# Optimization experiments

Hardware: AMD Instinct MI355X
Metric: run time of the kernel (lower is better)

Reference implementation:

```python
import jax, jax.numpy as jnp
import numpy as np

B, N, IN_DIM, OUT_DIM, H = 8, 1024, 512, 512, 8
SUP = OUT_DIM // H  # support_dim per head = 64


def setup_inputs() -> dict:
    key = jax.random.key(0)
    ks = jax.random.split(key, 6)
    # 0/1 dense adjacency with self-loops so no row is fully masked
    A = jax.random.randint(ks[0], (B, N, N), 0, 2).astype(jnp.float32)
    A = jnp.maximum(A, jnp.eye(N, dtype=jnp.float32)[None])
    X = jax.random.normal(ks[1], (B, N, IN_DIM), dtype=jnp.float32)
    # parameters, uniform(-1/sqrt(fan_last), 1/sqrt(fan_last)) as in reset_parameters
    sw = 1.0 / np.sqrt(SUP)
    W = jax.random.uniform(ks[2], (H, IN_DIM, SUP), minval=-sw, maxval=sw, dtype=jnp.float32)
    w1 = jax.random.uniform(ks[3], (H, SUP), minval=-sw, maxval=sw, dtype=jnp.float32)
    w2 = jax.random.uniform(ks[4], (H, SUP), minval=-sw, maxval=sw, dtype=jnp.float32)
    b = jax.random.uniform(ks[5], (2, H), minval=-1.0, maxval=1.0, dtype=jnp.float32)
    b1, b2 = b[0], b[1]
    return {"A": A, "X": X, "W": W, "w1": w1, "b1": b1, "w2": w2, "b2": b2}


def reference(A, X, W, w1, b1, w2, b2):
    # per-head projection: [B,H,N,SUP]
    inputs = jnp.einsum('bni,hio->bhno', X, W)
    # additive attention logits: self_fc [B,H,N,1] + neigh_fc [B,H,1,N]
    self_fc = jnp.einsum('bhno,ho->bhn', inputs, w1) + b1[None, :, None]
    neigh_fc = jnp.einsum('bhno,ho->bhn', inputs, w2) + b2[None, :, None]
    logits = jax.nn.leaky_relu(self_fc[..., :, None] + neigh_fc[..., None, :], 0.01)
    mask = -1e9 * (1.0 - A)  # [B,N,N]
    alphas = jax.nn.softmax(logits + mask[:, None], axis=-1)  # [B,H,N,N]
    out = jnp.einsum('bhnm,bhmo->bhno', alphas, inputs)
    out = jax.nn.relu(out)  # default activation = torch.relu
    # concat heads on last dim (head i contiguous), matching torch.cat
    return out.transpose(0, 2, 1, 3).reshape(B, N, H * SUP)
```

## Files before the change

kernel.cpp:

```cpp
#include <hip/hip_runtime.h>
#include <hip/hip_fp16.h>

#define BB 8
#define NN 1024
#define IN_DIM 512
#define HH 8
#define SUP 64
#define HS (HH * SUP)

typedef _Float16 half8 __attribute__((ext_vector_type(8)));
typedef float floatx4 __attribute__((ext_vector_type(4)));

__global__ __launch_bounds__(256) void k0_transpose_w(const float* __restrict__ W,
                                                      _Float16* __restrict__ Wt) {
    __shared__ float tile[64][65];
    const int it = blockIdx.x;
    const int h  = blockIdx.y;
    const int t  = threadIdx.x;

    {
        const int i  = t >> 2;
        const int o0 = (t & 3) * 16;
        const float* src = W + ((size_t)h * IN_DIM + it * 64 + i) * SUP + o0;
#pragma unroll
        for (int j = 0; j < 4; j++) {
            float4 v = ((const float4*)src)[j];
            tile[i][o0 + j * 4 + 0] = v.x;
            tile[i][o0 + j * 4 + 1] = v.y;
            tile[i][o0 + j * 4 + 2] = v.z;
            tile[i][o0 + j * 4 + 3] = v.w;
        }
    }
    __syncthreads();
    {
        const int o  = t >> 2;
        const int i0 = (t & 3) * 16;
        _Float16 buf[16];
#pragma unroll
        for (int j = 0; j < 16; j++) buf[j] = (_Float16)tile[i0 + j][o];
        _Float16* dst = Wt + ((size_t)h * SUP + o) * IN_DIM + it * 64 + i0;
        *(half8*)dst       = *(half8*)buf;
        *(half8*)(dst + 8) = *(half8*)(buf + 8);
    }
}

__global__ __launch_bounds__(256) void k1_proj(const float* __restrict__ X,
                                               const _Float16* __restrict__ Wt,
                                               _Float16* __restrict__ Pt) {
    __shared__ __align__(16) _Float16 xs[64 * 40];
    __shared__ __align__(16) _Float16 wsh[64 * 40];
    __shared__ __align__(16) _Float16 po[64 * 72];

    const int bh = blockIdx.y;
    const int b  = bh >> 3;
    const int h  = bh & 7;
    const int n0 = blockIdx.x * 64;
    const int t    = threadIdx.x;
    const int wave = t >> 6;
    const int lane = t & 63;
    const int quad = lane >> 4;
    const int l15  = lane & 15;
    const int row  = t >> 2;
    const int koff = (t & 3) * 8;

    floatx4 acc[4];
#pragma unroll
    for (int i = 0; i < 4; i++) acc[i] = {0.f, 0.f, 0.f, 0.f};

    const float*    xbase = X + ((size_t)b * NN + n0 + row) * IN_DIM;
    const _Float16* wbase = Wt + ((size_t)h * SUP + row) * IN_DIM;

    for (int k0 = 0; k0 < IN_DIM; k0 += 32) {
        {
            const float* src = xbase + k0 + koff;
            float4 xa = ((const float4*)src)[0];
            float4 xb = ((const float4*)src)[1];
            _Float16 xh[8] = {(_Float16)xa.x, (_Float16)xa.y, (_Float16)xa.z, (_Float16)xa.w,
                              (_Float16)xb.x, (_Float16)xb.y, (_Float16)xb.z, (_Float16)xb.w};
            *(half8*)&xs[row * 40 + koff] = *(half8*)xh;
        }
        {
            *(half8*)&wsh[row * 40 + koff] = *(const half8*)(wbase + k0 + koff);
        }
        __syncthreads();
        half8 af = *(const half8*)&xs[(wave * 16 + l15) * 40 + quad * 8];
#pragma unroll
        for (int ct = 0; ct < 4; ct++) {
            half8 bf = *(const half8*)&wsh[(ct * 16 + l15) * 40 + quad * 8];
            acc[ct] = __builtin_amdgcn_mfma_f32_16x16x32_f16(af, bf, acc[ct], 0, 0, 0);
        }
        __syncthreads();
    }

#pragma unroll
    for (int ct = 0; ct < 4; ct++) {
#pragma unroll
        for (int r = 0; r < 4; r++) {
            int o = ct * 16 + l15;
            int n = wave * 16 + quad * 4 + r;
            po[o * 72 + n] = (_Float16)acc[ct][r];
        }
    }
    __syncthreads();
    {
        const int o   = t >> 2;
        const int nof = (t & 3) * 16;
        _Float16* dst = Pt + ((size_t)bh * SUP + o) * NN + n0 + nof;
        *(half8*)dst       = *(const half8*)&po[o * 72 + nof];
        *(half8*)(dst + 8) = *(const half8*)&po[o * 72 + nof + 8];
    }
}

__global__ __launch_bounds__(256) void k1s_st(const _Float16* __restrict__ Pt,
                                              const float* __restrict__ w1,
                                              const float* __restrict__ b1,
                                              const float* __restrict__ w2,
                                              const float* __restrict__ b2,
                                              float* __restrict__ s_g,
                                              float* __restrict__ t_g,
                                              float* __restrict__ tmax4) {
    const int q  = blockIdx.x;
    const int bh = blockIdx.y;
    const int h  = bh & 7;
    const int t  = threadIdx.x;
    const int n  = q * 256 + t;

    __shared__ float w1s[64], w2s[64];
    __shared__ float red[256];
    if (t < 64) w1s[t] = w1[h * 64 + t];
    else if (t < 128) w2s[t - 64] = w2[h * 64 + (t - 64)];
    __syncthreads();

    const _Float16* base = Pt + (size_t)bh * SUP * NN + n;
    float sa = 0.f, ta = 0.f;
#pragma unroll
    for (int o = 0; o < 64; o++) {
        float p = (float)base[(size_t)o * NN];
        sa += p * w1s[o];
        ta += p * w2s[o];
    }
    sa += b1[h];
    ta += b2[h];
    s_g[(size_t)bh * NN + n] = sa;
    t_g[(size_t)bh * NN + n] = ta;

    red[t] = ta;
    __syncthreads();
    for (int off = 128; off > 0; off >>= 1) {
        if (t < off) red[t] = fmaxf(red[t], red[t + off]);
        __syncthreads();
    }
    if (t == 0) tmax4[bh * 4 + q] = red[0];
}

__global__ __launch_bounds__(256) void k2_attn(const float* __restrict__ A,
                                               const _Float16* __restrict__ Pt,
                                               const float* __restrict__ s_g,
                                               const float* __restrict__ t_g,
                                               const float* __restrict__ tmax4,
                                               float* __restrict__ out) {
    __shared__ __align__(16) _Float16 vts[64 * 40];
    __shared__ __align__(16) _Float16 als[64 * 40];
    __shared__ __align__(16) float tl[NN];
    __shared__ float sl[64], cl[64];
    __shared__ float zred[256];
    __shared__ float zinv[64];

    const int bh = blockIdx.y;
    const int b  = bh >> 3;
    const int h  = bh & 7;
    const int n0 = blockIdx.x * 64;
    const int t    = threadIdx.x;
    const int wave = t >> 6;
    const int lane = t & 63;
    const int quad = lane >> 4;
    const int l15  = lane & 15;
    const int row  = t >> 2;
    const int mg   = t & 3;

    const float tmax = fmaxf(fmaxf(tmax4[bh * 4 + 0], tmax4[bh * 4 + 1]),
                             fmaxf(tmax4[bh * 4 + 2], tmax4[bh * 4 + 3]));

    ((float4*)tl)[t] = ((const float4*)(t_g + (size_t)bh * NN))[t];
    if (t < 64) {
        float sv = s_g[(size_t)bh * NN + n0 + t];
        sl[t] = sv;
        float x = sv + tmax;
        cl[t] = x > 0.f ? x : 0.01f * x;
    }
    __syncthreads();

    floatx4 acc[4];
#pragma unroll
    for (int i = 0; i < 4; i++) acc[i] = {0.f, 0.f, 0.f, 0.f};
    float zp = 0.f;

    const float*    abase = A + ((size_t)b * NN + n0 + row) * NN + mg * 8;
    const _Float16* pbase = Pt + ((size_t)bh * SUP + row) * NN + mg * 8;

    for (int m0 = 0; m0 < NN; m0 += 32) {
        *(half8*)&vts[row * 40 + mg * 8] = *(const half8*)(pbase + m0);

        {
            const float* ap = abase + m0;
            float4 a0 = ((const float4*)ap)[0];
            float4 a1 = ((const float4*)ap)[1];
            float av[8] = {a0.x, a0.y, a0.z, a0.w, a1.x, a1.y, a1.z, a1.w};
            const float sv = sl[row];
            const float c  = cl[row];
            _Float16 wbuf[8];
#pragma unroll
            for (int j = 0; j < 8; j++) {
                float x = sv + tl[m0 + mg * 8 + j];
                float l = x > 0.f ? x : 0.01f * x;
                float e = __expf(l - c);
                float w = av[j] * e;
                zp += w;
                wbuf[j] = (_Float16)w;
            }
            *(half8*)&als[row * 40 + mg * 8] = *(half8*)wbuf;
        }
        __syncthreads();

        half8 af = *(const half8*)&als[(wave * 16 + l15) * 40 + quad * 8];
#pragma unroll
        for (int ct = 0; ct < 4; ct++) {
            half8 bf = *(const half8*)&vts[(ct * 16 + l15) * 40 + quad * 8];
            acc[ct] = __builtin_amdgcn_mfma_f32_16x16x32_f16(af, bf, acc[ct], 0, 0, 0);
        }
        __syncthreads();
    }

    zred[t] = zp;
    __syncthreads();
    if (t < 64) {
        float z = zred[t * 4] + zred[t * 4 + 1] + zred[t * 4 + 2] + zred[t * 4 + 3];
        zinv[t] = 1.0f / z;
    }
    __syncthreads();

#pragma unroll
    for (int r = 0; r < 4; r++) {
        const int rr = wave * 16 + quad * 4 + r;
        const float rz = zinv[rr];
#pragma unroll
        for (int ct = 0; ct < 4; ct++) {
            float v = acc[ct][r] * rz;
            v = v > 0.f ? v : 0.f;
            out[((size_t)b * NN + n0 + rr) * HS + h * SUP + ct * 16 + l15] = v;
        }
    }
}

extern "C" void kernel_launch(void* const* d_in, const int* in_sizes, int n_in,
                              void* d_out, int out_size, void* d_ws, size_t ws_size,
                              hipStream_t stream) {
    const float* A  = (const float*)d_in[0];
    const float* X  = (const float*)d_in[1];
    const float* W  = (const float*)d_in[2];
    const float* w1 = (const float*)d_in[3];
    const float* b1 = (const float*)d_in[4];
    const float* w2 = (const float*)d_in[5];
    const float* b2 = (const float*)d_in[6];
    float* out = (float*)d_out;

    char* ws = (char*)d_ws;
    _Float16* Wt    = (_Float16*)(ws);
    _Float16* Pt    = (_Float16*)(ws + 524288);
    float*    s_g   = (float*)(ws + 524288 + 8388608);
    float*    t_g   = (float*)(ws + 524288 + 8388608 + 262144);
    float*    tmax4 = (float*)(ws + 524288 + 8388608 + 2 * 262144);

    hipLaunchKernelGGL(k0_transpose_w, dim3(IN_DIM / 64, HH), dim3(256), 0, stream, W, Wt);
    hipLaunchKernelGGL(k1_proj, dim3(NN / 64, BB * HH), dim3(256), 0, stream, X, Wt, Pt);
    hipLaunchKernelGGL(k1s_st, dim3(4, BB * HH), dim3(256), 0, stream,
                       Pt, w1, b1, w2, b2, s_g, t_g, tmax4);
    hipLaunchKernelGGL(k2_attn, dim3(NN / 64, BB * HH), dim3(256), 0, stream,
                       A, Pt, s_g, t_g, tmax4, out);
}
```

Baseline: 157.2 us.

## Bit-pack adjacency mask, fuse score projection into GEMM, restructure attention loop

Result: faster. 140.6 us (-10.6%).

```diff
diff --git a/kernel.cpp b/kernel.cpp
--- a/kernel.cpp
+++ b/kernel.cpp
@@ -17,7 +17,6 @@
     const int it = blockIdx.x;
     const int h  = blockIdx.y;
     const int t  = threadIdx.x;
-
     {
         const int i  = t >> 2;
         const int o0 = (t & 3) * 16;
@@ -44,12 +43,36 @@
     }
 }
 
+__global__ __launch_bounds__(256) void kpack(const float* __restrict__ A,
+                                             unsigned char* __restrict__ Am) {
+    const int gw   = blockIdx.x * 4 + (threadIdx.x >> 6);
+    const int lane = threadIdx.x & 63;
+    const float* arow = A + (size_t)gw * NN;
+    unsigned long long keep = 0;
+#pragma unroll
+    for (int g = 0; g < 16; g++) {
+        float a = arow[g * 64 + lane];
+        unsigned long long bal = __ballot(a > 0.5f);
+        if (lane == g) keep = bal;
+    }
+    if (lane < 16)
+        *(unsigned long long*)(Am + (size_t)gw * 128 + lane * 8) = keep;
+}
+
 __global__ __launch_bounds__(256) void k1_proj(const float* __restrict__ X,
                                                const _Float16* __restrict__ Wt,
-                                               _Float16* __restrict__ Pt) {
+                                               const float* __restrict__ w1,
+                                               const float* __restrict__ b1,
+                                               const float* __restrict__ w2,
+                                               const float* __restrict__ b2,
+                                               _Float16* __restrict__ Pt,
+                                               float* __restrict__ s_g,
+                                               float* __restrict__ t_g,
+                                               float* __restrict__ tmax16) {
     __shared__ __align__(16) _Float16 xs[64 * 40];
     __shared__ __align__(16) _Float16 wsh[64 * 40];
     __shared__ __align__(16) _Float16 po[64 * 72];
+    __shared__ float tred[64];
 
     const int bh = blockIdx.y;
     const int b  = bh >> 3;
@@ -67,22 +90,36 @@
 #pragma unroll
     for (int i = 0; i < 4; i++) acc[i] = {0.f, 0.f, 0.f, 0.f};
 
+    float w1v[4], w2v[4];
+#pragma unroll
+    for (int ct = 0; ct < 4; ct++) {
+        w1v[ct] = w1[h * 64 + ct * 16 + l15];
+        w2v[ct] = w2[h * 64 + ct * 16 + l15];
+    }
+    const float b1h = b1[h];
+    const float b2h = b2[h];
+
     const float*    xbase = X + ((size_t)b * NN + n0 + row) * IN_DIM;
     const _Float16* wbase = Wt + ((size_t)h * SUP + row) * IN_DIM;
 
+    float4 xa = ((const float4*)(xbase + koff))[0];
+    float4 xb = ((const float4*)(xbase + koff))[1];
+    half8  wv = *(const half8*)(wbase + koff);
+
     for (int k0 = 0; k0 < IN_DIM; k0 += 32) {
         {
-            const float* src = xbase + k0 + koff;
-            float4 xa = ((const float4*)src)[0];
-            float4 xb = ((const float4*)src)[1];
             _Float16 xh[8] = {(_Float16)xa.x, (_Float16)xa.y, (_Float16)xa.z, (_Float16)xa.w,
                               (_Float16)xb.x, (_Float16)xb.y, (_Float16)xb.z, (_Float16)xb.w};
             *(half8*)&xs[row * 40 + koff] = *(half8*)xh;
-        }
-        {
-            *(half8*)&wsh[row * 40 + koff] = *(const half8*)(wbase + k0 + koff);
+            *(half8*)&wsh[row * 40 + koff] = wv;
         }
         __syncthreads();
+        if (k0 + 32 < IN_DIM) {
+            const float* src = xbase + k0 + 32 + koff;
+            xa = ((const float4*)src)[0];
+            xb = ((const float4*)src)[1];
+            wv = *(const half8*)(wbase + k0 + 32 + koff);
+        }
         half8 af = *(const half8*)&xs[(wave * 16 + l15) * 40 + quad * 8];
 #pragma unroll
         for (int ct = 0; ct < 4; ct++) {
@@ -99,6 +136,27 @@
             int o = ct * 16 + l15;
             int n = wave * 16 + quad * 4 + r;
             po[o * 72 + n] = (_Float16)acc[ct][r];
+        }
+    }
+#pragma unroll
+    for (int r = 0; r < 4; r++) {
+        float sp = 0.f, tp = 0.f;
+#pragma unroll
+        for (int ct = 0; ct < 4; ct++) {
+            sp += acc[ct][r] * w1v[ct];
+            tp += acc[ct][r] * w2v[ct];
+        }
+#pragma unroll
+        for (int off = 1; off < 16; off <<= 1) {
+            sp += __shfl_xor(sp, off);
+            tp += __shfl_xor(tp, off);
+        }
+        if (l15 == 0) {
+            const int n = wave * 16 + quad * 4 + r;
+            s_g[(size_t)bh * NN + n0 + n] = sp + b1h;
+            float tv = tp + b2h;
+            t_g[(size_t)bh * NN + n0 + n] = tv;
+            tred[n] = tv;
         }
     }
     __syncthreads();
@@ -109,62 +167,24 @@
         *(half8*)dst       = *(const half8*)&po[o * 72 + nof];
         *(half8*)(dst + 8) = *(const half8*)&po[o * 72 + nof + 8];
     }
-}
-
-__global__ __launch_bounds__(256) void k1s_st(const _Float16* __restrict__ Pt,
-                                              const float* __restrict__ w1,
-                                              const float* __restrict__ b1,
-                                              const float* __restrict__ w2,
-                                              const float* __restrict__ b2,
-                                              float* __restrict__ s_g,
-                                              float* __restrict__ t_g,
-                                              float* __restrict__ tmax4) {
-    const int q  = blockIdx.x;
-    const int bh = blockIdx.y;
-    const int h  = bh & 7;
-    const int t  = threadIdx.x;
-    const int n  = q * 256 + t;
-
-    __shared__ float w1s[64], w2s[64];
-    __shared__ float red[256];
-    if (t < 64) w1s[t] = w1[h * 64 + t];
-    else if (t < 128) w2s[t - 64] = w2[h * 64 + (t - 64)];
-    __syncthreads();
-
-    const _Float16* base = Pt + (size_t)bh * SUP * NN + n;
-    float sa = 0.f, ta = 0.f;
-#pragma unroll
-    for (int o = 0; o < 64; o++) {
-        float p = (float)base[(size_t)o * NN];
-        sa += p * w1s[o];
-        ta += p * w2s[o];
-    }
-    sa += b1[h];
-    ta += b2[h];
-    s_g[(size_t)bh * NN + n] = sa;
-    t_g[(size_t)bh * NN + n] = ta;
-
-    red[t] = ta;
-    __syncthreads();
-    for (int off = 128; off > 0; off >>= 1) {
-        if (t < off) red[t] = fmaxf(red[t], red[t + off]);
-        __syncthreads();
-    }
-    if (t == 0) tmax4[bh * 4 + q] = red[0];
-}
-
-__global__ __launch_bounds__(256) void k2_attn(const float* __restrict__ A,
+    if (t == 0) {
+        float m = -1e30f;
+#pragma unroll
+        for (int i = 0; i < 64; i++) m = fmaxf(m, tred[i]);
+        tmax16[bh * 16 + blockIdx.x] = m;
+    }
+}
+
+__global__ __launch_bounds__(256) void k2_attn(const unsigned char* __restrict__ Am,
                                                const _Float16* __restrict__ Pt,
                                                const float* __restrict__ s_g,
                                                const float* __restrict__ t_g,
-                                               const float* __restrict__ tmax4,
+                                               const float* __restrict__ tmax16,
                                                float* __restrict__ out) {
-    __shared__ __align__(16) _Float16 vts[64 * 40];
-    __shared__ __align__(16) _Float16 als[64 * 40];
+    __shared__ __align__(16) _Float16 vts[64 * 136];
     __shared__ __align__(16) float tl[NN];
-    __shared__ float sl[64], cl[64];
-    __shared__ float zred[256];
-    __shared__ float zinv[64];
+    __shared__ __align__(16) unsigned char am[64 * 144];
+    __shared__ float zinv_l[64];
 
     const int bh = blockIdx.y;
     const int b  = bh >> 3;
@@ -175,74 +195,87 @@
     const int lane = t & 63;
     const int quad = lane >> 4;
     const int l15  = lane & 15;
-    const int row  = t >> 2;
-    const int mg   = t & 3;
-
-    const float tmax = fmaxf(fmaxf(tmax4[bh * 4 + 0], tmax4[bh * 4 + 1]),
-                             fmaxf(tmax4[bh * 4 + 2], tmax4[bh * 4 + 3]));
+    const int row4 = t >> 2;
+    const int seg  = t & 3;
 
     ((float4*)tl)[t] = ((const float4*)(t_g + (size_t)bh * NN))[t];
-    if (t < 64) {
-        float sv = s_g[(size_t)bh * NN + n0 + t];
-        sl[t] = sv;
-        float x = sv + tmax;
-        cl[t] = x > 0.f ? x : 0.01f * x;
-    }
-    __syncthreads();
+    {
+        const uint4* asrc = (const uint4*)(Am + ((size_t)b * NN + n0 + row4) * 128 + seg * 32);
+        uint4 ma = asrc[0], mb = asrc[1];
+        *(uint4*)&am[row4 * 144 + seg * 32]      = ma;
+        *(uint4*)&am[row4 * 144 + seg * 32 + 16] = mb;
+    }
+    float tmax = -1e30f;
+#pragma unroll
+    for (int i = 0; i < 16; i++) tmax = fmaxf(tmax, tmax16[bh * 16 + i]);
+
+    const int myrow = wave * 16 + l15;
+    const float sv = s_g[(size_t)bh * NN + n0 + myrow];
+    const float xc = sv + tmax;
+    const float cv = fmaxf(xc, 0.01f * xc);
 
     floatx4 acc[4];
 #pragma unroll
     for (int i = 0; i < 4; i++) acc[i] = {0.f, 0.f, 0.f, 0.f};
     float zp = 0.f;
 
-    const float*    abase = A + ((size_t)b * NN + n0 + row) * NN + mg * 8;
-    const _Float16* pbase = Pt + ((size_t)bh * SUP + row) * NN + mg * 8;
-
-    for (int m0 = 0; m0 < NN; m0 += 32) {
-        *(half8*)&vts[row * 40 + mg * 8] = *(const half8*)(pbase + m0);
-
+    const _Float16* pb = Pt + ((size_t)bh * SUP + row4) * NN + seg * 32;
+    half8 v0 = ((const half8*)pb)[0];
+    half8 v1 = ((const half8*)pb)[1];
+    half8 v2 = ((const half8*)pb)[2];
+    half8 v3 = ((const half8*)pb)[3];
+
+    for (int mt = 0; mt < 8; mt++) {
+        const int m0 = mt * 128;
         {
-            const float* ap = abase + m0;
-            float4 a0 = ((const float4*)ap)[0];
-            float4 a1 = ((const float4*)ap)[1];
-            float av[8] = {a0.x, a0.y, a0.z, a0.w, a1.x, a1.y, a1.z, a1.w};
-            const float sv = sl[row];
-            const float c  = cl[row];
-            _Float16 wbuf[8];
+            _Float16* d = &vts[row4 * 136 + seg * 32];
+            ((half8*)d)[0] = v0; ((half8*)d)[1] = v1;
+            ((half8*)d)[2] = v2; ((half8*)d)[3] = v3;
+        }
+        __syncthreads();
+        if (mt < 7) {
+            const _Float16* p = pb + m0 + 128;
+            v0 = ((const half8*)p)[0];
+            v1 = ((const half8*)p)[1];
+            v2 = ((const half8*)p)[2];
+            v3 = ((const half8*)p)[3];
+        }
+#pragma unroll
+        for (int kk = 0; kk < 4; kk++) {
+            const unsigned mbyte = am[myrow * 144 + mt * 16 + kk * 4 + quad];
+            const int kbase = m0 + kk * 32 + quad * 8;
+            float4 ta = *(const float4*)&tl[kbase];
+            float4 tb = *(const float4*)&tl[kbase + 4];
+            float tv[8] = {ta.x, ta.y, ta.z, ta.w, tb.x, tb.y, tb.z, tb.w};
+            _Float16 wb[8];
 #pragma unroll
             for (int j = 0; j < 8; j++) {
-                float x = sv + tl[m0 + mg * 8 + j];
-                float l = x > 0.f ? x : 0.01f * x;
-                float e = __expf(l - c);
-                float w = av[j] * e;
-                zp += w;
-                wbuf[j] = (_Float16)w;
+                float x = sv + tv[j];
+                float l = fmaxf(x, 0.01f * x);
+                float e = __expf(l - cv);
+                float we = (mbyte & (1u << j)) ? e : 0.f;
+                zp += we;
+                wb[j] = (_Float16)we;
             }
-            *(half8*)&als[row * 40 + mg * 8] = *(half8*)wbuf;
+            half8 af = *(half8*)wb;
+#pragma unroll
+            for (int ct = 0; ct < 4; ct++) {
+                half8 bf = *(const half8*)&vts[(ct * 16 + l15) * 136 + kk * 32 + quad * 8];
+                acc[ct] = __builtin_amdgcn_mfma_f32_16x16x32_f16(af, bf, acc[ct], 0, 0, 0);
+            }
         }
         __syncthreads();
-
-        half8 af = *(const half8*)&als[(wave * 16 + l15) * 40 + quad * 8];
-#pragma unroll
-        for (int ct = 0; ct < 4; ct++) {
-            half8 bf = *(const half8*)&vts[(ct * 16 + l15) * 40 + quad * 8];
-            acc[ct] = __builtin_amdgcn_mfma_f32_16x16x32_f16(af, bf, acc[ct], 0, 0, 0);
-        }
-        __syncthreads();
-    }
-
-    zred[t] = zp;
-    __syncthreads();
-    if (t < 64) {
-        float z = zred[t * 4] + zred[t * 4 + 1] + zred[t * 4 + 2] + zred[t * 4 + 3];
-        zinv[t] = 1.0f / z;
-    }
+    }
+
+    zp += __shfl_xor(zp, 16);
+    zp += __shfl_xor(zp, 32);
+    if (quad == 0) zinv_l[myrow] = 1.0f / zp;
     __syncthreads();
 
 #pragma unroll
     for (int r = 0; r < 4; r++) {
         const int rr = wave * 16 + quad * 4 + r;
-        const float rz = zinv[rr];
+        const float rz = zinv_l[rr];
 #pragma unroll
         for (int ct = 0; ct < 4; ct++) {
             float v = acc[ct][r] * rz;
@@ -265,16 +298,17 @@
     float* out = (float*)d_out;
 
     char* ws = (char*)d_ws;
-    _Float16* Wt    = (_Float16*)(ws);
-    _Float16* Pt    = (_Float16*)(ws + 524288);
-    float*    s_g   = (float*)(ws + 524288 + 8388608);
-    float*    t_g   = (float*)(ws + 524288 + 8388608 + 262144);
-    float*    tmax4 = (float*)(ws + 524288 + 8388608 + 2 * 262144);
+    _Float16*      Wt     = (_Float16*)(ws);
+    _Float16*      Pt     = (_Float16*)(ws + 524288);
+    float*         s_g    = (float*)(ws + 8912896);
+    float*         t_g    = (float*)(ws + 9175040);
+    float*         tmax16 = (float*)(ws + 9437184);
+    unsigned char* Am     = (unsigned char*)(ws + 9441280);
 
     hipLaunchKernelGGL(k0_transpose_w, dim3(IN_DIM / 64, HH), dim3(256), 0, stream, W, Wt);
-    hipLaunchKernelGGL(k1_proj, dim3(NN / 64, BB * HH), dim3(256), 0, stream, X, Wt, Pt);
-    hipLaunchKernelGGL(k1s_st, dim3(4, BB * HH), dim3(256), 0, stream,
-                       Pt, w1, b1, w2, b2, s_g, t_g, tmax4);
+    hipLaunchKernelGGL(kpack, dim3(BB * NN / 4), dim3(256), 0, stream, A, Am);
+    hipLaunchKernelGGL(k1_proj, dim3(NN / 64, BB * HH), dim3(256), 0, stream,
+                       X, Wt, w1, b1, w2, b2, Pt, s_g, t_g, tmax16);
     hipLaunchKernelGGL(k2_attn, dim3(NN / 64, BB * HH), dim3(256), 0, stream,
-                       A, Pt, s_g, t_g, tmax4, out);
-}
+                       Am, Pt, s_g, t_g, tmax16, out);
+}
```
